# Kernel optimization log

Hardware: AMD Instinct MI355X
Metric: run time of the kernel (lower is better)

The kernel has to match this reference:

```python
import jax, jax.numpy as jnp
import numpy as np

B, S, C = 2, 2048, 1536
HQ, HKV = 16, 4
DQK, DV = 128, 96
MAX_POS = 2048
CLIP = 5.0
EPS = 1e-5


def layer_norm(x, g, b):
    mu = jnp.mean(x, axis=-1, keepdims=True)
    var = jnp.mean(jnp.square(x - mu), axis=-1, keepdims=True)
    return (x - mu) * jax.lax.rsqrt(var + EPS) * g + b


def rms_bn(x, g, ms):
    # eval-mode EMA RMS batch-norm: per-channel running mean-square `ms`
    return x * jax.lax.rsqrt(ms + EPS) * g


def rope(x):
    # x: [B, S, H, C] with C even
    c = x.shape[-1]
    nf = c // 2
    s = x.shape[1]
    positions = jnp.arange(s, dtype=x.dtype)
    lin = jnp.arange(nf, dtype=x.dtype)
    end = max(MAX_POS - nf + 1.0, 1.0)
    geom = jnp.exp(jnp.linspace(0.0, jnp.log(jnp.asarray(end, dtype=x.dtype)), nf))
    inv_freq = 1.0 / (lin + geom)
    theta = positions[:, None] * inv_freq          # [S, nf]
    theta = jnp.repeat(theta, 2, axis=-1)[:, None, :]  # [S, 1, C]
    x_rot = jnp.stack([-x[..., 1::2], x[..., ::2]], axis=-1).reshape(x.shape)
    return x * jnp.cos(theta) + x_rot * jnp.sin(theta)


def setup_inputs() -> dict:
    key = jax.random.key(0)
    ks = jax.random.split(key, 8)
    d = {
        'x': jax.random.normal(ks[0], (B, S, C), dtype=jnp.float32),
        'bn1_g': jnp.ones((C,), jnp.float32),
        'bn1_ms': jnp.ones((C,), jnp.float32),
        'Wq': jax.random.normal(ks[1], (C, HQ * DQK), jnp.float32) * 0.02,
        'Wk': jax.random.normal(ks[2], (C, HKV * DQK), jnp.float32) * 0.02,
        'Wv': jax.random.normal(ks[3], (C, HKV * DV), jnp.float32) * 0.02,
        'qn_g': jnp.ones((DQK,), jnp.float32), 'qn_b': jnp.zeros((DQK,), jnp.float32),
        'kn_g': jnp.ones((DQK,), jnp.float32), 'kn_b': jnp.zeros((DQK,), jnp.float32),
        'vn_g': jnp.ones((DV,), jnp.float32), 'vn_b': jnp.zeros((DV,), jnp.float32),
        'Wo': jax.random.normal(ks[4], (HQ * DV, C), jnp.float32) * 0.02,
        'bo': jnp.zeros((C,), jnp.float32),
        'bn2_g': jnp.ones((C,), jnp.float32),
        'bn2_ms': jnp.ones((C,), jnp.float32),
    }
    return d


def reference(x, bn1_g, bn1_ms, Wq, Wk, Wv, qn_g, qn_b, kn_g, kn_b, vn_g, vn_b, Wo, bo, bn2_g, bn2_ms):
    rep = HQ // HKV
    h = rms_bn(x, bn1_g, bn1_ms)                       # [B,S,C]
    q = (h @ Wq).reshape(B, S, HQ, DQK)
    k = (h @ Wk).reshape(B, S, HKV, DQK)
    v = (h @ Wv).reshape(B, S, HKV, DV)
    q = layer_norm(q, qn_g, qn_b)
    k = layer_norm(k, kn_g, kn_b)
    v = layer_norm(v, vn_g, vn_b)
    q = rope(q)
    k = rope(k)
    # torch .repeat(1,1,rep,1) tiles head axis: [h0..hkv-1] * rep
    k = jnp.tile(k, (1, 1, rep, 1))                    # [B,S,HQ,DQK]
    v = jnp.tile(v, (1, 1, rep, 1))                    # [B,S,HQ,DV]
    logits = jnp.einsum('bshc,bShc->bhsS', q, k) / (DQK ** 0.5)
    logits = jnp.tanh(logits / CLIP) * CLIP
    attn = jax.nn.softmax(logits, axis=-1)
    y = jnp.einsum('bhsS,bShc->bshc', attn, v)         # [B,S,HQ,DV]
    y = y.reshape(B, S, HQ * DV)
    y = y @ Wo + bo
    y = rms_bn(y, bn2_g, bn2_ms)
    return y
```

## Files before the change

kernel.cpp:

```cpp
#include <hip/hip_runtime.h>
#include <hip/hip_bf16.h>
#include <math.h>

typedef __hip_bfloat16 bf16;
typedef __attribute__((ext_vector_type(8))) short short8;
typedef __attribute__((ext_vector_type(4))) short short4s;
typedef __attribute__((ext_vector_type(4))) float f32x4;

constexpr int Bb=2, Ss=2048, Cc=1536, HQn=16, HKVn=4, Dqk=128, Dv=96;
constexpr int NR   = Bb*Ss;
constexpr int NQKV = HQn*Dqk + HKVn*Dqk + HKVn*Dv;
constexpr int COL_K = HQn*Dqk;
constexpr int COL_V = COL_K + HKVn*Dqk;
constexpr int NY   = HQn*Dv;
constexpr float EPSf=1e-5f, CLIPf=5.0f;
constexpr float LOG2E = 1.44269504089f;

__device__ __forceinline__ float s2f(short s) {
    unsigned u = ((unsigned)(unsigned short)s) << 16;
    return __builtin_bit_cast(float, u);
}
__device__ __forceinline__ short f2s(float v) {
    bf16 b = __float2bfloat16(v);
    return __builtin_bit_cast(short, b);
}
__device__ __forceinline__ bool is_bf(const void* tagp) {
    return ((*(const unsigned*)tagp) & 0xFFFFu) != 0u;
}
__device__ __forceinline__ float ldd(const void* p, size_t i, bool bf) {
    return bf ? s2f(((const short*)p)[i]) : ((const float*)p)[i];
}

__global__ __launch_bounds__(256) void k_pre(const void* g1, const void* ms1,
        const void* bo, const void* g2, const void* ms2,
        float* __restrict__ ascale, float* __restrict__ ebias,
        float* __restrict__ escale, float2* __restrict__ tab) {
    bool bf = is_bf(ms1);
    int idx = blockIdx.x*256 + threadIdx.x;
    if (idx < Cc) {
        ascale[idx] = rsqrtf(ldd(ms1,idx,bf) + EPSf) * ldd(g1,idx,bf);
        ebias[idx]  = ldd(bo,idx,bf);
        escale[idx] = rsqrtf(ldd(ms2,idx,bf) + EPSf) * ldd(g2,idx,bf);
    }
    if (idx < Ss*64) {
        int s = idx >> 6, f = idx & 63;
        float geom = expf((float)f * (logf(1985.0f) * (1.0f/63.0f)));
        float invf = 1.0f / ((float)f + geom);
        float th = (float)s * invf;
        tab[idx] = make_float2(cosf(th), sinf(th));
    }
}

__global__ __launch_bounds__(256) void k_bn1(const void* __restrict__ x,
        const float* __restrict__ ascale, short* __restrict__ h, const void* tagp) {
    bool bf = is_bf(tagp);
    size_t i8 = (size_t)(blockIdx.x*256 + threadIdx.x) * 8;
    if (i8 >= (size_t)NR*Cc) return;
    int c = (int)(i8 % Cc);
    float xv[8];
    if (bf) {
        short8 xa = *(const short8*)((const short*)x + i8);
        #pragma unroll
        for (int j=0;j<8;++j) xv[j] = s2f(xa[j]);
    } else {
        const float* xf = (const float*)x + i8;
        #pragma unroll
        for (int j=0;j<8;++j) xv[j] = xf[j];
    }
    short8 o;
    #pragma unroll
    for (int j=0;j<8;++j) o[j] = f2s(xv[j] * ascale[c+j]);
    *(short8*)(h + i8) = o;
}

__global__ __launch_bounds__(256) void k_trw(const void* __restrict__ Wq,
        const void* __restrict__ Wk, const void* __restrict__ Wv,
        const void* __restrict__ Wo, short* __restrict__ WT, const void* tagp) {
    __shared__ short tile[32][33];
    bool bf = is_bf(tagp);
    int gt = blockIdx.x*32;
    int k0 = blockIdx.y*32;
    const void* W; int N, nl;
    if      (gt < 2048) { W = Wq; N = 2048; nl = gt; }
    else if (gt < 2560) { W = Wk; N = 512;  nl = gt - 2048; }
    else if (gt < 2944) { W = Wv; N = 384;  nl = gt - 2560; }
    else                { W = Wo; N = 1536; nl = gt - 2944; }
    int t = threadIdx.x, c = t & 31;
    #pragma unroll
    for (int r8=0; r8<32; r8+=8) {
        int r = r8 + (t>>5);
        tile[r][c] = f2s(ldd(W, (size_t)(k0+r)*N + nl + c, bf));
    }
    __syncthreads();
    #pragma unroll
    for (int r8=0; r8<32; r8+=8) {
        int r = r8 + (t>>5);
        WT[(size_t)(gt + r)*Cc + k0 + c] = tile[c][r];
    }
}

__global__ __launch_bounds__(256) void k_gemm(const short* __restrict__ A,
        const short* __restrict__ BT, void* __restrict__ Cout,
        int M, int N, int K,
        const float* __restrict__ ebias, const float* __restrict__ escale,
        int epi, const void* tagp) {
    __shared__ short As[128*32];
    __shared__ short Bs[128*32];
    const int t = threadIdx.x;
    const int w = t >> 6, lane = t & 63;
    const int l15 = lane & 15, quad = lane >> 4;
    const int wm = (w>>1)*64, wn = (w&1)*64;
    const int m0 = blockIdx.y*128, n0 = blockIdx.x*128;
    const int c0 = lane >> 2;
    const int koff = (lane & 3) * 8;

    f32x4 acc[4][4];
    #pragma unroll
    for (int i=0;i<4;++i)
        #pragma unroll
        for (int j=0;j<4;++j) acc[i][j] = (f32x4){0.f,0.f,0.f,0.f};

    for (int k0 = 0; k0 < K; k0 += 32) {
        __syncthreads();
        #pragma unroll
        for (int c=0; c<2; ++c) {
            int rA = w*32 + c*16;
            const short* ga = A  + (size_t)(m0 + rA + c0)*K + k0 + koff;
            const short* gb = BT + (size_t)(n0 + rA + c0)*K + k0 + koff;
            __builtin_amdgcn_global_load_lds(
                (const __attribute__((address_space(1))) void*)ga,
                (__attribute__((address_space(3))) void*)&As[rA*32], 16, 0, 0);
            __builtin_amdgcn_global_load_lds(
                (const __attribute__((address_space(1))) void*)gb,
                (__attribute__((address_space(3))) void*)&Bs[rA*32], 16, 0, 0);
        }
        __syncthreads();
        short8 af[4], bfr[4];
        #pragma unroll
        for (int mt=0; mt<4; ++mt)
            af[mt] = *(const short8*)&As[(wm + mt*16 + l15)*32 + quad*8];
        #pragma unroll
        for (int nt=0; nt<4; ++nt)
            bfr[nt] = *(const short8*)&Bs[(wn + nt*16 + l15)*32 + quad*8];
        #pragma unroll
        for (int mt=0; mt<4; ++mt)
            #pragma unroll
            for (int nt=0; nt<4; ++nt)
                acc[mt][nt] = __builtin_amdgcn_mfma_f32_16x16x32_bf16(
                    af[mt], bfr[nt], acc[mt][nt], 0, 0, 0);
    }

    const bool outf32 = epi && !is_bf(tagp);
    #pragma unroll
    for (int mt=0; mt<4; ++mt) {
        #pragma unroll
        for (int nt=0; nt<4; ++nt) {
            int col = n0 + wn + nt*16 + l15;
            float eb = epi ? ebias[col]  : 0.f;
            float es = epi ? escale[col] : 1.f;
            #pragma unroll
            for (int reg=0; reg<4; ++reg) {
                int row = m0 + wm + mt*16 + quad*4 + reg;
                float v = acc[mt][nt][reg];
                if (epi) v = (v + eb) * es;
                if (outf32) ((float*)Cout)[(size_t)row*N + col] = v;
                else        ((short*)Cout)[(size_t)row*N + col] = f2s(v);
            }
        }
    }
}

__global__ __launch_bounds__(256) void k_ln(short* __restrict__ qkvb,
        const float2* __restrict__ tab,
        const void* qg, const void* qb_, const void* kg, const void* kb_,
        const void* vg, const void* vb_, const void* tagp) {
    bool bf = is_bf(tagp);
    int R = blockIdx.x*4 + (threadIdx.x>>6);
    int lane = threadIdx.x & 63;
    int hidx = R % 24, bs = R / 24, s = bs % Ss;
    const void *g, *bia; int coff, D, dorope;
    if (hidx < 16)      { coff = hidx*Dqk;              D = Dqk; g = qg; bia = qb_; dorope = 1; }
    else if (hidx < 20) { coff = COL_K + (hidx-16)*Dqk; D = Dqk; g = kg; bia = kb_; dorope = 1; }
    else                { coff = COL_V + (hidx-20)*Dv;  D = Dv;  g = vg; bia = vb_; dorope = 0; }
    short* p = qkvb + (size_t)bs*NQKV + coff;
    int d0 = lane*2;
    bool act = d0 < D;
    float v0 = 0.f, v1 = 0.f;
    if (act) { v0 = s2f(p[d0]); v1 = s2f(p[d0+1]); }
    float sum = v0 + v1;
    #pragma unroll
    for (int m=1; m<64; m<<=1) sum += __shfl_xor(sum, m);
    float mu = sum / (float)D;
    float c0 = act ? v0-mu : 0.f, c1 = act ? v1-mu : 0.f;
    float sq = c0*c0 + c1*c1;
    #pragma unroll
    for (int m=1; m<64; m<<=1) sq += __shfl_xor(sq, m);
    float r = rsqrtf(sq/(float)D + EPSf);
    if (act) {
        float y0 = c0*r*ldd(g,d0,bf)   + ldd(bia,d0,bf);
        float y1 = c1*r*ldd(g,d0+1,bf) + ldd(bia,d0+1,bf);
        if (dorope) {
            float2 cs = tab[s*64 + lane];
            float t0 = y0*cs.x - y1*cs.y;
            y1 = y1*cs.x + y0*cs.y;
            y0 = t0;
        }
        p[d0] = f2s(y0); p[d0+1] = f2s(y1);
    }
}

__global__ __launch_bounds__(256) void k_trv(const short* __restrict__ qkvb,
        short* __restrict__ vT) {
    __shared__ short tile[32][33];
    int bs0 = blockIdx.x*32;
    int dg0 = blockIdx.y*32;
    int t = threadIdx.x, c = t & 31;
    #pragma unroll
    for (int r8=0; r8<32; r8+=8) {
        int r = r8 + (t>>5);
        tile[r][c] = qkvb[(size_t)(bs0+r)*NQKV + COL_V + dg0 + c];
    }
    __syncthreads();
    int b = bs0 >> 11, s0 = bs0 & 2047;
    int s = s0 + c;
    int sp = (s & ~63) + ((s>>5)&1)*32 + ((s>>2)&3)*8 + ((s>>4)&1)*4 + (s&3);
    #pragma unroll
    for (int r8=0; r8<32; r8+=8) {
        int r = r8 + (t>>5);
        vT[((size_t)(b*384 + dg0 + r))*Ss + sp] = tile[c][r];
    }
}

__global__ __launch_bounds__(256) void k_attn(const short* __restrict__ qkvb,
        const short* __restrict__ vT, short* __restrict__ Yb) {
    __shared__ __align__(16) short Ks[2][64*136];
    __shared__ __align__(16) short VTs[2][96*72];
    const int wg = blockIdx.x;
    const int xcd = wg & 7, idx = wg >> 3;
    const int b = xcd >> 2, kvh = xcd & 3;
    const int qb = idx >> 2, hsub = idx & 3;
    const int hq = hsub*4 + kvh;
    const int q0 = qb*128;
    const int t = threadIdx.x;
    const int w = t >> 6, lane = t & 63;
    const int l15 = lane & 15, quad = lane >> 4;
    const float ctan = 2.0f * (0.0883883476f / CLIPf) * LOG2E;
    const float c2   = -2.0f * CLIPf * LOG2E;

    short8 qf[2][4];
    #pragma unroll
    for (int qt=0; qt<2; ++qt) {
        const short* qp = qkvb + (size_t)(b*Ss + q0 + w*32 + qt*16 + l15)*NQKV + hq*Dqk;
        #pragma unroll
        for (int ds=0; ds<4; ++ds) qf[qt][ds] = *(const short8*)(qp + ds*32 + quad*8);
    }

    f32x4 oacc[2][6];
    #pragma unroll
    for (int qt=0; qt<2; ++qt)
        #pragma unroll
        for (int nt=0; nt<6; ++nt) oacc[qt][nt] = (f32x4){0.f,0.f,0.f,0.f};
    float lsum[2] = {0.f, 0.f};

    const short* Kb = qkvb + ((size_t)b*Ss)*NQKV + COL_K + kvh*Dqk;
    const short* Vb = vT + ((size_t)(b*HKVn + kvh)*Dv)*Ss;

    short8 kreg[4], vreg[3];
    auto stage_load = [&](int j0) {
        #pragma unroll
        for (int it=0; it<4; ++it) {
            int ii = it*256 + t;
            kreg[it] = *(const short8*)(Kb + (size_t)(j0 + (ii>>4))*NQKV + (ii&15)*8);
        }
        #pragma unroll
        for (int it=0; it<3; ++it) {
            int ii = it*256 + t;
            vreg[it] = *(const short8*)(Vb + (size_t)(ii>>3)*Ss + j0 + (ii&7)*8);
        }
    };
    auto stage_write = [&](int pb) {
        #pragma unroll
        for (int it=0; it<4; ++it) {
            int ii = it*256 + t;
            *(short8*)&Ks[pb][(ii>>4)*136 + (ii&15)*8] = kreg[it];
        }
        #pragma unroll
        for (int it=0; it<3; ++it) {
            int ii = it*256 + t;
            *(short8*)&VTs[pb][(ii>>3)*72 + (ii&7)*8] = vreg[it];
        }
    };

    stage_load(0);
    stage_write(0);
    int p = 0;
    constexpr int NCH = Ss/64;
    for (int kc = 0; kc < NCH; ++kc) {
        __syncthreads();
        if (kc+1 < NCH) stage_load((kc+1)*64);

        f32x4 sacc[4][2];
        #pragma unroll
        for (int kt=0; kt<4; ++kt)
            #pragma unroll
            for (int qt=0; qt<2; ++qt) sacc[kt][qt] = (f32x4){0.f,0.f,0.f,0.f};
        __builtin_amdgcn_s_setprio(1);
        #pragma unroll
        for (int kt=0; kt<4; ++kt) {
            short8 kf[4];
            #pragma unroll
            for (int ds=0; ds<4; ++ds)
                kf[ds] = *(const short8*)&Ks[p][(kt*16 + l15)*136 + ds*32 + quad*8];
            #pragma unroll
            for (int qt=0; qt<2; ++qt)
                #pragma unroll
                for (int ds=0; ds<4; ++ds)
                    sacc[kt][qt] = __builtin_amdgcn_mfma_f32_16x16x32_bf16(
                        kf[ds], qf[qt][ds], sacc[kt][qt], 0, 0, 0);
        }
        __builtin_amdgcn_s_setprio(0);

        short8 pa[2][2];
        #pragma unroll
        for (int c=0; c<2; ++c)
            #pragma unroll
            for (int qt=0; qt<2; ++qt)
                #pragma unroll
                for (int jh=0; jh<2; ++jh)
                    #pragma unroll
                    for (int j=0; j<4; ++j) {
                        float u  = __builtin_amdgcn_exp2f(sacc[c*2+jh][qt][j] * ctan);
                        float pv = __builtin_amdgcn_exp2f(c2 * __builtin_amdgcn_rcpf(u + 1.0f));
                        short ps = f2s(pv);
                        pa[c][qt][jh*4 + j] = ps;
                        lsum[qt] += s2f(ps);
                    }

        __builtin_amdgcn_s_setprio(1);
        #pragma unroll
        for (int c=0; c<2; ++c)
            #pragma unroll
            for (int nt=0; nt<6; ++nt) {
                short8 vf = *(const short8*)&VTs[p][(nt*16 + l15)*72 + c*32 + quad*8];
                #pragma unroll
                for (int qt=0; qt<2; ++qt)
                    oacc[qt][nt] = __builtin_amdgcn_mfma_f32_16x16x32_bf16(
                        pa[c][qt], vf, oacc[qt][nt], 0, 0, 0);
            }
        __builtin_amdgcn_s_setprio(0);

        if (kc+1 < NCH) stage_write(p^1);
        p ^= 1;
    }

    float lred[2];
    #pragma unroll
    for (int qt=0; qt<2; ++qt) {
        float l = lsum[qt];
        l += __shfl_xor(l, 16);
        l += __shfl_xor(l, 32);
        lred[qt] = l;
    }
    #pragma unroll
    for (int qt=0; qt<2; ++qt) {
        float rinv[4];
        #pragma unroll
        for (int reg=0; reg<4; ++reg)
            rinv[reg] = __builtin_amdgcn_rcpf(__shfl(lred[qt], quad*4 + reg, 16));
        #pragma unroll
        for (int nt=0; nt<6; ++nt)
            #pragma unroll
            for (int reg=0; reg<4; ++reg) {
                int row = q0 + w*32 + qt*16 + quad*4 + reg;
                Yb[(size_t)(b*Ss + row)*NY + hq*Dv + nt*16 + l15] =
                    f2s(oacc[qt][nt][reg] * rinv[reg]);
            }
    }
}

extern "C" void kernel_launch(void* const* d_in, const int* in_sizes, int n_in,
                              void* d_out, int out_size, void* d_ws, size_t ws_size,
                              hipStream_t stream) {
    const void* x     = d_in[0];
    const void* bn1g  = d_in[1];
    const void* bn1ms = d_in[2];
    const void* Wq    = d_in[3];
    const void* Wk    = d_in[4];
    const void* Wv    = d_in[5];
    const void* qng   = d_in[6];
    const void* qnb   = d_in[7];
    const void* kng   = d_in[8];
    const void* knb   = d_in[9];
    const void* vng   = d_in[10];
    const void* vnb   = d_in[11];
    const void* Wo    = d_in[12];
    const void* bo    = d_in[13];
    const void* bn2g  = d_in[14];
    const void* bn2ms = d_in[15];

    char* wsb = (char*)d_ws;
    float*  ascale = (float*)(wsb);
    float*  ebias  = (float*)(wsb + 6144);
    float*  escale = (float*)(wsb + 12288);
    float2* tab    = (float2*)(wsb + 18432);
    short*  h      = (short*)(wsb + 1067520);
    short*  WT     = (short*)(wsb + 13650432);
    short*  qkv    = (short*)(wsb + 27412992);
    short*  vT     = (short*)(wsb + 51530240);
    short*  y      = (short*)(wsb + 54675968);
    short*  WoT    = WT + (size_t)NQKV*Cc;

    k_pre<<<512, 256, 0, stream>>>(bn1g, bn1ms, bo, bn2g, bn2ms,
                                   ascale, ebias, escale, tab);
    k_bn1<<<(NR*Cc/8 + 255)/256, 256, 0, stream>>>(x, ascale, h, bn1ms);
    k_trw<<<dim3(4480/32, Cc/32), 256, 0, stream>>>(Wq, Wk, Wv, Wo, WT, bn1ms);

    k_gemm<<<dim3(NQKV/128, NR/128), 256, 0, stream>>>(
        h, WT, qkv, NR, NQKV, Cc, nullptr, nullptr, 0, bn1ms);

    k_ln<<<NR*24/4, 256, 0, stream>>>(qkv, tab, qng, qnb, kng, knb, vng, vnb, bn1ms);
    k_trv<<<dim3(NR/32, 384/32), 256, 0, stream>>>(qkv, vT);

    k_attn<<<512, 256, 0, stream>>>(qkv, vT, y);

    k_gemm<<<dim3(Cc/128, NR/128), 256, 0, stream>>>(
        y, WoT, d_out, NR, Cc, NY, ebias, escale, 1, bn1ms);
}
```

Baseline: 355.8 us.

## Split attention KV chunk across two wave halves with async LDS loads

The attention kernel goes from 256 to 512 threads. Two groups of four waves each take half of every 64-key chunk for the same query rows, and their partial outputs and row sums are combined through shared memory at the end. K/V staging switches from register round-trips to direct global-to-LDS loads into XOR-swizzled, unpadded tiles. The aim is more waves per block to hide latency and fewer VGPRs and instructions for staging, at the cost of a final cross-half reduction and an extra barrier.

```diff
diff --git a/kernel.cpp b/kernel.cpp
--- a/kernel.cpp
+++ b/kernel.cpp
@@ -29,6 +29,11 @@
 }
 __device__ __forceinline__ float ldd(const void* p, size_t i, bool bf) {
     return bf ? s2f(((const short*)p)[i]) : ((const float*)p)[i];
+}
+__device__ __forceinline__ void gll16(const void* src, void* lds) {
+    __builtin_amdgcn_global_load_lds(
+        (const __attribute__((address_space(1))) void*)src,
+        (__attribute__((address_space(3))) void*)lds, 16, 0, 0);
 }
 
 __global__ __launch_bounds__(256) void k_pre(const void* g1, const void* ms1,
@@ -127,12 +132,8 @@
             int rA = w*32 + c*16;
             const short* ga = A  + (size_t)(m0 + rA + c0)*K + k0 + koff;
             const short* gb = BT + (size_t)(n0 + rA + c0)*K + k0 + koff;
-            __builtin_amdgcn_global_load_lds(
-                (const __attribute__((address_space(1))) void*)ga,
-                (__attribute__((address_space(3))) void*)&As[rA*32], 16, 0, 0);
-            __builtin_amdgcn_global_load_lds(
-                (const __attribute__((address_space(1))) void*)gb,
-                (__attribute__((address_space(3))) void*)&Bs[rA*32], 16, 0, 0);
+            gll16(ga, &As[rA*32]);
+            gll16(gb, &Bs[rA*32]);
         }
         __syncthreads();
         short8 af[4], bfr[4];
@@ -231,10 +232,11 @@
     }
 }
 
-__global__ __launch_bounds__(256) void k_attn(const short* __restrict__ qkvb,
+__global__ __launch_bounds__(512, 4) void k_attn(const short* __restrict__ qkvb,
         const short* __restrict__ vT, short* __restrict__ Yb) {
-    __shared__ __align__(16) short Ks[2][64*136];
-    __shared__ __align__(16) short VTs[2][96*72];
+    __shared__ __align__(16) short smem[2*64*128 + 2*96*64];
+    auto Ks  = (short(*)[64*128])smem;
+    auto VTs = (short(*)[96*64])(smem + 2*64*128);
     const int wg = blockIdx.x;
     const int xcd = wg & 7, idx = wg >> 3;
     const int b = xcd >> 2, kvh = xcd & 3;
@@ -243,14 +245,41 @@
     const int q0 = qb*128;
     const int t = threadIdx.x;
     const int w = t >> 6, lane = t & 63;
+    const int qw = w & 3, half = w >> 2;
     const int l15 = lane & 15, quad = lane >> 4;
+    const int xr = (l15 & 7) * 16;
     const float ctan = 2.0f * (0.0883883476f / CLIPf) * LOG2E;
     const float c2   = -2.0f * CLIPf * LOG2E;
 
+    const short* Kb = qkvb + ((size_t)b*Ss)*NQKV + COL_K + kvh*Dqk;
+    const short* Vb = vT + ((size_t)(b*HKVn + kvh)*Dv)*Ss;
+
+    const int rK = 4*w + (lane>>4);
+    const char* kq0 = (const char*)Kb + (size_t)rK*NQKV*2
+                    + (((lane&15)*16) ^ ((rK&7)*16));
+    const int dv0 = 8*w + (lane>>3);
+    const char* vq0 = (const char*)Vb + (size_t)dv0*Ss*2
+                    + (((lane&7)*16) ^ ((dv0&7)*16));
+    const size_t KADV = (size_t)64*NQKV*2;
+    const size_t KOFF2 = (size_t)32*NQKV*2;
+    const size_t VOFF2 = (size_t)64*Ss*2;
+
+    auto issue_stage = [&](int pb) {
+        char* KD = (char*)&Ks[pb][0];
+        char* VD = (char*)&VTs[pb][0];
+        gll16(kq0,         KD + w*1024);
+        gll16(kq0 + KOFF2, KD + (w+8)*1024);
+        gll16(vq0,         VD + w*1024);
+        if (w < 4) gll16(vq0 + VOFF2, VD + (w+8)*1024);
+        kq0 += KADV; vq0 += 128;
+    };
+
+    issue_stage(0);
+
     short8 qf[2][4];
     #pragma unroll
     for (int qt=0; qt<2; ++qt) {
-        const short* qp = qkvb + (size_t)(b*Ss + q0 + w*32 + qt*16 + l15)*NQKV + hq*Dqk;
+        const short* qp = qkvb + (size_t)(b*Ss + q0 + qw*32 + qt*16 + l15)*NQKV + hq*Dqk;
         #pragma unroll
         for (int ds=0; ds<4; ++ds) qf[qt][ds] = *(const short8*)(qp + ds*32 + quad*8);
     }
@@ -262,119 +291,105 @@
         for (int nt=0; nt<6; ++nt) oacc[qt][nt] = (f32x4){0.f,0.f,0.f,0.f};
     float lsum[2] = {0.f, 0.f};
 
-    const short* Kb = qkvb + ((size_t)b*Ss)*NQKV + COL_K + kvh*Dqk;
-    const short* Vb = vT + ((size_t)(b*HKVn + kvh)*Dv)*Ss;
-
-    short8 kreg[4], vreg[3];
-    auto stage_load = [&](int j0) {
-        #pragma unroll
-        for (int it=0; it<4; ++it) {
-            int ii = it*256 + t;
-            kreg[it] = *(const short8*)(Kb + (size_t)(j0 + (ii>>4))*NQKV + (ii&15)*8);
-        }
-        #pragma unroll
-        for (int it=0; it<3; ++it) {
-            int ii = it*256 + t;
-            vreg[it] = *(const short8*)(Vb + (size_t)(ii>>3)*Ss + j0 + (ii&7)*8);
-        }
-    };
-    auto stage_write = [&](int pb) {
-        #pragma unroll
-        for (int it=0; it<4; ++it) {
-            int ii = it*256 + t;
-            *(short8*)&Ks[pb][(ii>>4)*136 + (ii&15)*8] = kreg[it];
-        }
-        #pragma unroll
-        for (int it=0; it<3; ++it) {
-            int ii = it*256 + t;
-            *(short8*)&VTs[pb][(ii>>3)*72 + (ii&7)*8] = vreg[it];
-        }
-    };
-
-    stage_load(0);
-    stage_write(0);
     int p = 0;
     constexpr int NCH = Ss/64;
     for (int kc = 0; kc < NCH; ++kc) {
         __syncthreads();
-        if (kc+1 < NCH) stage_load((kc+1)*64);
-
-        f32x4 sacc[4][2];
-        #pragma unroll
-        for (int kt=0; kt<4; ++kt)
-            #pragma unroll
-            for (int qt=0; qt<2; ++qt) sacc[kt][qt] = (f32x4){0.f,0.f,0.f,0.f};
+        if (kc+1 < NCH) issue_stage(p^1);
+
+        const char* KsB  = (const char*)&Ks[p][0];
+        const char* VTsB = (const char*)&VTs[p][0];
+
+        short8 pa[2];
+        #pragma unroll
+        for (int kt=0; kt<2; ++kt) {
+            const int r = (half*2 + kt)*16 + l15;
+            const char* krow = KsB + r*256;
+            short8 kf[4];
+            #pragma unroll
+            for (int ds=0; ds<4; ++ds)
+                kf[ds] = *(const short8*)(krow + ((ds*64 + quad*16) ^ xr));
+            f32x4 s0 = (f32x4){0.f,0.f,0.f,0.f}, s1 = (f32x4){0.f,0.f,0.f,0.f};
+            __builtin_amdgcn_s_setprio(1);
+            #pragma unroll
+            for (int ds=0; ds<4; ++ds) {
+                s0 = __builtin_amdgcn_mfma_f32_16x16x32_bf16(kf[ds], qf[0][ds], s0, 0, 0, 0);
+                s1 = __builtin_amdgcn_mfma_f32_16x16x32_bf16(kf[ds], qf[1][ds], s1, 0, 0, 0);
+            }
+            __builtin_amdgcn_s_setprio(0);
+            #pragma unroll
+            for (int j=0; j<4; ++j) {
+                float u0 = __builtin_amdgcn_exp2f(s0[j] * ctan);
+                float p0 = __builtin_amdgcn_exp2f(c2 * __builtin_amdgcn_rcpf(u0 + 1.0f));
+                short ps0 = f2s(p0);
+                pa[0][kt*4+j] = ps0; lsum[0] += s2f(ps0);
+                float u1 = __builtin_amdgcn_exp2f(s1[j] * ctan);
+                float p1 = __builtin_amdgcn_exp2f(c2 * __builtin_amdgcn_rcpf(u1 + 1.0f));
+                short ps1 = f2s(p1);
+                pa[1][kt*4+j] = ps1; lsum[1] += s2f(ps1);
+            }
+        }
+
         __builtin_amdgcn_s_setprio(1);
         #pragma unroll
-        for (int kt=0; kt<4; ++kt) {
-            short8 kf[4];
-            #pragma unroll
-            for (int ds=0; ds<4; ++ds)
-                kf[ds] = *(const short8*)&Ks[p][(kt*16 + l15)*136 + ds*32 + quad*8];
-            #pragma unroll
-            for (int qt=0; qt<2; ++qt)
+        for (int nt=0; nt<6; ++nt) {
+            const int dvrow = nt*16 + l15;
+            short8 vf = *(const short8*)(VTsB + dvrow*128 + ((half*64 + quad*16) ^ xr));
+            oacc[0][nt] = __builtin_amdgcn_mfma_f32_16x16x32_bf16(pa[0], vf, oacc[0][nt], 0, 0, 0);
+            oacc[1][nt] = __builtin_amdgcn_mfma_f32_16x16x32_bf16(pa[1], vf, oacc[1][nt], 0, 0, 0);
+        }
+        __builtin_amdgcn_s_setprio(0);
+        p ^= 1;
+    }
+
+    __syncthreads();
+    float* red = (float*)smem;
+    const int rbase = (qw*64 + lane)*52;
+    if (half == 1) {
+        #pragma unroll
+        for (int qt=0; qt<2; ++qt)
+            #pragma unroll
+            for (int nt=0; nt<6; ++nt)
+                *(f32x4*)&red[rbase + (qt*6+nt)*4] = oacc[qt][nt];
+        red[rbase+48] = lsum[0];
+        red[rbase+49] = lsum[1];
+    }
+    __syncthreads();
+    if (half == 0) {
+        #pragma unroll
+        for (int qt=0; qt<2; ++qt)
+            #pragma unroll
+            for (int nt=0; nt<6; ++nt) {
+                f32x4 o = *(const f32x4*)&red[rbase + (qt*6+nt)*4];
                 #pragma unroll
-                for (int ds=0; ds<4; ++ds)
-                    sacc[kt][qt] = __builtin_amdgcn_mfma_f32_16x16x32_bf16(
-                        kf[ds], qf[qt][ds], sacc[kt][qt], 0, 0, 0);
-        }
-        __builtin_amdgcn_s_setprio(0);
-
-        short8 pa[2][2];
-        #pragma unroll
-        for (int c=0; c<2; ++c)
-            #pragma unroll
-            for (int qt=0; qt<2; ++qt)
+                for (int j=0;j<4;++j) oacc[qt][nt][j] += o[j];
+            }
+        lsum[0] += red[rbase+48];
+        lsum[1] += red[rbase+49];
+
+        float lred[2];
+        #pragma unroll
+        for (int qt=0; qt<2; ++qt) {
+            float l = lsum[qt];
+            l += __shfl_xor(l, 16);
+            l += __shfl_xor(l, 32);
+            lred[qt] = l;
+        }
+        #pragma unroll
+        for (int qt=0; qt<2; ++qt) {
+            float rinv[4];
+            #pragma unroll
+            for (int reg=0; reg<4; ++reg)
+                rinv[reg] = __builtin_amdgcn_rcpf(__shfl(lred[qt], quad*4 + reg, 16));
+            #pragma unroll
+            for (int nt=0; nt<6; ++nt)
                 #pragma unroll
-                for (int jh=0; jh<2; ++jh)
-                    #pragma unroll
-                    for (int j=0; j<4; ++j) {
-                        float u  = __builtin_amdgcn_exp2f(sacc[c*2+jh][qt][j] * ctan);
-                        float pv = __builtin_amdgcn_exp2f(c2 * __builtin_amdgcn_rcpf(u + 1.0f));
-                        short ps = f2s(pv);
-                        pa[c][qt][jh*4 + j] = ps;
-                        lsum[qt] += s2f(ps);
-                    }
-
-        __builtin_amdgcn_s_setprio(1);
-        #pragma unroll
-        for (int c=0; c<2; ++c)
-            #pragma unroll
-            for (int nt=0; nt<6; ++nt) {
-                short8 vf = *(const short8*)&VTs[p][(nt*16 + l15)*72 + c*32 + quad*8];
-                #pragma unroll
-                for (int qt=0; qt<2; ++qt)
-                    oacc[qt][nt] = __builtin_amdgcn_mfma_f32_16x16x32_bf16(
-                        pa[c][qt], vf, oacc[qt][nt], 0, 0, 0);
-            }
-        __builtin_amdgcn_s_setprio(0);
-
-        if (kc+1 < NCH) stage_write(p^1);
-        p ^= 1;
-    }
-
-    float lred[2];
-    #pragma unroll
-    for (int qt=0; qt<2; ++qt) {
-        float l = lsum[qt];
-        l += __shfl_xor(l, 16);
-        l += __shfl_xor(l, 32);
-        lred[qt] = l;
-    }
-    #pragma unroll
-    for (int qt=0; qt<2; ++qt) {
-        float rinv[4];
-        #pragma unroll
-        for (int reg=0; reg<4; ++reg)
-            rinv[reg] = __builtin_amdgcn_rcpf(__shfl(lred[qt], quad*4 + reg, 16));
-        #pragma unroll
-        for (int nt=0; nt<6; ++nt)
-            #pragma unroll
-            for (int reg=0; reg<4; ++reg) {
-                int row = q0 + w*32 + qt*16 + quad*4 + reg;
-                Yb[(size_t)(b*Ss + row)*NY + hq*Dv + nt*16 + l15] =
-                    f2s(oacc[qt][nt][reg] * rinv[reg]);
-            }
+                for (int reg=0; reg<4; ++reg) {
+                    int row = q0 + qw*32 + qt*16 + quad*4 + reg;
+                    Yb[(size_t)(b*Ss + row)*NY + hq*Dv + nt*16 + l15] =
+                        f2s(oacc[qt][nt][reg] * rinv[reg]);
+                }
+        }
     }
 }
 
@@ -421,7 +436,7 @@
     k_ln<<<NR*24/4, 256, 0, stream>>>(qkv, tab, qng, qnb, kng, knb, vng, vnb, bn1ms);
     k_trv<<<dim3(NR/32, 384/32), 256, 0, stream>>>(qkv, vT);
 
-    k_attn<<<512, 256, 0, stream>>>(qkv, vT, y);
+    k_attn<<<512, 512, 0, stream>>>(qkv, vT, y);
 
     k_gemm<<<dim3(Cc/128, NR/128), 256, 0, stream>>>(
         y, WoT, d_out, NR, Cc, NY, ebias, escale, 1, bn1ms);
```

Result: faster. 345.6 us (-2.9%).
